# Optimization experiments

Measured on AMD Instinct MI355X. Metric: run time of the kernel, lower is better.

Reference implementation:

```python
import jax, jax.numpy as jnp
import numpy as np

HEADS = 8
NEG_SLOPE = 0.2


def _leaky(x):
    return jnp.where(x >= 0, x, NEG_SLOPE * x)


def _layernorm(x, g, b):
    # torch nn.LayerNorm over last dim, eps=1e-5, biased variance
    m = x.mean(-1, keepdims=True)
    v = ((x - m) ** 2).mean(-1, keepdims=True)
    return (x - m) / jnp.sqrt(v + 1e-5) * g + b


def _batchnorm(x, g, b):
    # training-mode BatchNorm2d, eps=1e-4, biased variance over (N,H,W)
    m = x.mean((0, 2, 3), keepdims=True)
    v = ((x - m) ** 2).mean((0, 2, 3), keepdims=True)
    return (x - m) / jnp.sqrt(v + 1e-4) * g[None, :, None, None] + b[None, :, None, None]


def _depthwise3x3(x, k):
    # x: (B,C,H,W), k: (C,1,3,3) depthwise kernel
    C = x.shape[1]
    return jax.lax.conv_general_dilated(
        x, k, (1, 1), 'SAME', feature_group_count=C,
        dimension_numbers=('NCHW', 'OIHW', 'NCHW'))


def _attn_layer(x, wq, wk, wv, wproj, bproj, wpos):
    # x: (B,H,W,C) channels-last; MDTA-style transposed attention
    b, H, W, C = x.shape
    d = C // HEADS
    xf = x.reshape(b, H * W, C)
    q, k, v = xf @ wq, xf @ wk, xf @ wv  # (b, n, C)

    def split(t):
        return t.reshape(b, H * W, HEADS, d).transpose(0, 2, 3, 1)  # (b, h, d, n)

    qh, kh, vh = split(q), split(k), split(v)
    # F.normalize over token axis n (eps=1e-12)
    qn = qh / jnp.maximum(jnp.sqrt((qh * qh).sum(-1, keepdims=True)), 1e-12)
    kn = kh / jnp.maximum(jnp.sqrt((kh * kh).sum(-1, keepdims=True)), 1e-12)
    attn = jax.nn.softmax(jnp.einsum('bhdn,bhen->bhde', kn, qn), axis=-1)  # (b,h,d,d)
    o = jnp.einsum('bhde,bhen->bhdn', attn, vh)  # (b,h,d,n)
    o = o.transpose(0, 3, 1, 2).reshape(b, H * W, C)
    out_c = (o @ wproj + bproj).reshape(b, H, W, C)
    out_p = _depthwise3x3(v.reshape(b, H, W, C).transpose(0, 3, 1, 2), wpos).transpose(0, 2, 3, 1)
    return out_c * out_p


def _transformer_block(x, wq, wk, wv, wproj, bproj, wpos, ln_g, ln_b, wff):
    # x: NCHW -> BHWC, 2 (attn + prenorm-FF) residual blocks, -> NCHW
    x = x.transpose(0, 2, 3, 1)
    for i in range(wq.shape[0]):
        x = _attn_layer(x, wq[i], wk[i], wv[i], wproj[i], bproj[i], wpos[i]) + x
        x = _layernorm(x, ln_g[i], ln_b[i]) @ wff[i] + x
    return x.transpose(0, 3, 1, 2)


def _saa(x, w1, w2):
    # SAA_Block: 8x8 spatial pool, global min-max norm, bmm correlation, SE gating
    b, c, H, W = x.shape
    y = x.reshape(b, c, 8, H // 8, 8, W // 8).mean((3, 5)).reshape(b, c, 64)
    y = (y - y.min()) / (y.max() - y.min())
    y = jnp.einsum('bci,bdi->bcd', y, y).mean(2)[:, :, None, None]  # (b,c,1,1)
    g = (x * y).mean((2, 3))  # (b,c) global avg pool
    g = jax.nn.sigmoid(_leaky(g @ w1) @ w2)
    return x * g[:, :, None, None]


def setup_inputs() -> dict:
    key = jax.random.key(0)
    B, C, H, W = 16, 64, 128, 128
    L = 2  # num_blocks in Transformer_block
    ks = jax.random.split(key, 12)
    s = 0.05
    inp = {
        'x': jax.random.normal(ks[0], (B, C, H, W), jnp.float32),
        'wq': jax.random.normal(ks[1], (L, C, C), jnp.float32) * s,
        'wk': jax.random.normal(ks[2], (L, C, C), jnp.float32) * s,
        'wv': jax.random.normal(ks[3], (L, C, C), jnp.float32) * s,
        'wproj': jax.random.normal(ks[4], (L, C, C), jnp.float32) * s,
        'bproj': jnp.zeros((L, C), jnp.float32),
        'wpos': jax.random.normal(ks[5], (L, C, 1, 3, 3), jnp.float32) * s,
        'ln_g': jnp.ones((L, C), jnp.float32),
        'ln_b': jnp.zeros((L, C), jnp.float32),
        'wff': jax.random.normal(ks[6], (L, C, C), jnp.float32) * s,
        'bn1_g': jnp.ones((C,), jnp.float32),
        'bn1_b': jnp.zeros((C,), jnp.float32),
        'wd': jax.random.normal(ks[7], (C, C), jnp.float32) * s,
        'bn2_g': jnp.ones((C,), jnp.float32),
        'bn2_b': jnp.zeros((C,), jnp.float32),
        'saa_w1': jax.random.normal(ks[8], (C, C // 16), jnp.float32) * s,
        'saa_w2': jax.random.normal(ks[9], (C // 16, C), jnp.float32) * s,
    }
    return inp


def reference(x, wq, wk, wv, wproj, bproj, wpos, ln_g, ln_b, wff,
              bn1_g, bn1_b, wd, bn2_g, bn2_b, saa_w1, saa_w2):
    # res path: C (Transformer_block) -> L -> B -> D (1x1 conv) -> L -> B
    r = _transformer_block(x, wq, wk, wv, wproj, bproj, wpos, ln_g, ln_b, wff)
    r = _batchnorm(_leaky(r), bn1_g, bn1_b)
    r = jnp.einsum('bchw,co->bohw', r, wd)  # 1x1 conv, bias=False
    r = _batchnorm(_leaky(r), bn2_g, bn2_b)
    return _saa(r + x, saa_w1, saa_w2)
```

## Files before the change

kernel.cpp:

```cpp
#include <hip/hip_runtime.h>

constexpr int NB = 16, NC = 64, NH = 128, NW = 128;
constexpr int NPIX = NH * NW;
constexpr int NTOT = NB * NPIX;
constexpr size_t BUF = (size_t)NTOT * NC;

constexpr size_t OFF_A   = 0;
constexpr size_t OFF_ACT = BUF;
constexpr size_t OFF_V   = 2 * BUF;
constexpr size_t OFF_S   = 3 * BUF;
constexpr size_t OFF_QSQ = OFF_S   + 2*16*512;
constexpr size_t OFF_KSQ = OFF_QSQ + 2048;
constexpr size_t OFF_BN1 = OFF_KSQ + 2048;
constexpr size_t OFF_BN2 = OFF_BN1 + 128;
constexpr size_t ZERO_FLOATS = 16384 + 2048 + 2048 + 128 + 128;
constexpr size_t OFF_W2  = OFF_BN2 + 128;
constexpr size_t OFF_AB1 = OFF_W2  + 131072;
constexpr size_t OFF_AB2 = OFF_AB1 + 128;
constexpr size_t OFF_Y   = OFF_AB2 + 128;
constexpr size_t OFF_GATE= OFF_Y   + 65536;

__device__ __forceinline__ float leaky(float x) { return x >= 0.f ? x : 0.2f * x; }
#define RFL __builtin_amdgcn_readfirstlane

__global__ __launch_bounds__(256) void k_transpose_in(const float* __restrict__ x,
                                                      float* __restrict__ A) {
  __shared__ float t[64][65];
  int blk = blockIdx.x;
  int b = blk >> 8;
  int p0 = (blk & 255) * 64;
  int tid = threadIdx.x;
  int cq = tid >> 6, p = tid & 63;
  for (int i = 0; i < 16; i++) {
    int c = cq * 16 + i;
    t[p][c] = x[((size_t)(b * 64 + c)) * NPIX + p0 + p];
  }
  __syncthreads();
  int pq = tid >> 6, c = tid & 63;
  for (int i = 0; i < 16; i++) {
    int p2 = pq * 16 + i;
    A[((size_t)(b * NPIX + p0 + p2)) * 64 + c] = t[p2][c];
  }
}

__global__ __launch_bounds__(256, 2) void k_qkv(const float* __restrict__ act,
    const float* __restrict__ wq, const float* __restrict__ wk,
    const float* __restrict__ wv, float* __restrict__ v,
    float* __restrict__ S, float* __restrict__ qsq, float* __restrict__ ksq,
    int l) {
  __shared__ float xb[8][64];
  int tid = threadIdx.x;
  int lane = tid & 63;
  int wid = RFL((int)(blockIdx.x * 4 + (tid >> 6)));
  int wslot = wid & 3;
  int b = wid >> 8;
  const float* Wq = wq + (size_t)l * 4096;
  const float* Wk = wk + (size_t)l * 4096;
  const float* Wv = wv + (size_t)l * 4096;
  float wqc[64], wkc[64], wvc[64];
#pragma unroll
  for (int ci = 0; ci < 64; ci++) {
    wqc[ci] = Wq[ci * 64 + lane];
    wkc[ci] = Wk[ci * 64 + lane];
    wvc[ci] = Wv[ci * 64 + lane];
  }
  float Sacc[8];
#pragma unroll
  for (int e = 0; e < 8; e++) Sacc[e] = 0.f;
  float qsa = 0.f, ksa = 0.f;
  int gbase = lane & 56;
  int base = wid * 4096;
#pragma unroll 1
  for (int p = 0; p < 64; p++) {
    int off = base + p * 64;
    float xl = act[off + lane];
    int xs = wslot * 2 + (p & 1);
    xb[xs][lane] = xl;
    const float4* x4p = (const float4*)xb[xs];
    float q = 0.f, k = 0.f, vv = 0.f;
#pragma unroll
    for (int i = 0; i < 16; i++) {
      float4 x4 = x4p[i];
      q  = fmaf(x4.x, wqc[4*i+0], q);
      k  = fmaf(x4.x, wkc[4*i+0], k);
      vv = fmaf(x4.x, wvc[4*i+0], vv);
      q  = fmaf(x4.y, wqc[4*i+1], q);
      k  = fmaf(x4.y, wkc[4*i+1], k);
      vv = fmaf(x4.y, wvc[4*i+1], vv);
      q  = fmaf(x4.z, wqc[4*i+2], q);
      k  = fmaf(x4.z, wkc[4*i+2], k);
      vv = fmaf(x4.z, wvc[4*i+2], vv);
      q  = fmaf(x4.w, wqc[4*i+3], q);
      k  = fmaf(x4.w, wkc[4*i+3], k);
      vv = fmaf(x4.w, wvc[4*i+3], vv);
    }
    qsa = fmaf(q, q, qsa);
    ksa = fmaf(k, k, ksa);
#pragma unroll
    for (int e = 0; e < 8; e++) {
      float qe = __shfl(q, gbase + e, 64);
      Sacc[e] = fmaf(k, qe, Sacc[e]);
    }
    v[off + lane] = vv;
  }
  float* Sb = S + ((size_t)l * 16 + b) * 512 + lane * 8;
#pragma unroll
  for (int e = 0; e < 8; e++) atomicAdd(Sb + e, Sacc[e]);
  atomicAdd(qsq + ((size_t)l * 16 + b) * 64 + lane, qsa);
  atomicAdd(ksq + ((size_t)l * 16 + b) * 64 + lane, ksa);
}

__global__ __launch_bounds__(64) void k_attn(const float* __restrict__ S,
    const float* __restrict__ qsq, const float* __restrict__ ksq,
    const float* __restrict__ wproj, float* __restrict__ W2, int l) {
  int b = blockIdx.x, t = threadIdx.x;
  __shared__ float A[8][8][8];
  const float* Sb = S + ((size_t)l * 16 + b) * 512;
  const float* qs = qsq + ((size_t)l * 16 + b) * 64;
  const float* ks = ksq + ((size_t)l * 16 + b) * 64;
  int h = t >> 3, d = t & 7;
  float kden = fmaxf(sqrtf(ks[h * 8 + d]), 1e-12f);
  float pre[8];
  float mx = -1e30f;
#pragma unroll
  for (int e = 0; e < 8; e++) {
    float qden = fmaxf(sqrtf(qs[h * 8 + e]), 1e-12f);
    pre[e] = Sb[(h * 8 + d) * 8 + e] / (kden * qden);
    mx = fmaxf(mx, pre[e]);
  }
  float sum = 0.f;
#pragma unroll
  for (int e = 0; e < 8; e++) { pre[e] = expf(pre[e] - mx); sum += pre[e]; }
  float inv = 1.f / sum;
#pragma unroll
  for (int e = 0; e < 8; e++) A[h][d][e] = pre[e] * inv;
  __syncthreads();
  int co = t;
  const float* wp = wproj + (size_t)l * 4096;
  float* W2b = W2 + ((size_t)l * 16 + b) * 4096;
#pragma unroll 1
  for (int cin = 0; cin < 64; cin++) {
    int hh2 = cin >> 3, e = cin & 7;
    float acc = 0.f;
#pragma unroll
    for (int dd = 0; dd < 8; dd++)
      acc = fmaf(A[hh2][dd][e], wp[(hh2 * 8 + dd) * 64 + co], acc);
    W2b[cin * 64 + co] = acc;
  }
}

__global__ __launch_bounds__(256, 2) void k_attnout_ff(
    const float* __restrict__ vbuf, const float* __restrict__ actin,
    float* __restrict__ actout, const float* __restrict__ W2all,
    const float* __restrict__ bproj, const float* __restrict__ wpos,
    const float* __restrict__ lng, const float* __restrict__ lnb,
    const float* __restrict__ wff, float* __restrict__ bn1, int l, int dobn) {
  __shared__ float xb[8][64], yb[8][64];
  int tid = threadIdx.x;
  int lane = tid & 63;
  int bid = blockIdx.x;
  int sbid = (bid & 7) * 128 + (bid >> 3);
  int wid = RFL((int)(sbid * 4 + (tid >> 6)));
  int wslot = wid & 3;
  int b = wid >> 8;
  int widb = wid & 255;
  int hh = widb >> 1;
  int c0 = (widb & 1) * 64;
  const float* W2 = W2all + ((size_t)l * 16 + b) * 4096;
  const float* WF = wff + (size_t)l * 4096;
  float w2c[64], wfc[64];
#pragma unroll
  for (int ci = 0; ci < 64; ci++) {
    w2c[ci] = W2[ci * 64 + lane];
    wfc[ci] = WF[ci * 64 + lane];
  }
  float wpc[9];
#pragma unroll
  for (int kk = 0; kk < 9; kk++) wpc[kk] = wpos[(size_t)l * 576 + lane * 9 + kk];
  float bp = bproj[l * 64 + lane];
  float G  = lng[l * 64 + lane];
  float Bb = lnb[l * 64 + lane];

  bool okm = (hh > 0), okp = (hh < 127);
  int base = wid * 4096;
  float Lm = 0.f, L0 = 0.f, Lp = 0.f, Cm = 0.f, C0, Cp = 0.f;
  C0 = vbuf[base + lane];
  if (okm) Cm = vbuf[base - 8192 + lane];
  if (okp) Cp = vbuf[base + 8192 + lane];
  if (c0 == 64) {
    L0 = vbuf[base - 64 + lane];
    if (okm) Lm = vbuf[base - 64 - 8192 + lane];
    if (okp) Lp = vbuf[base - 64 + 8192 + lane];
  }
  float s_bn = 0.f, s2_bn = 0.f;
#pragma unroll 1
  for (int p = 0; p < 64; p++) {
    int off = base + p * 64;
    float Rm = 0.f, R0 = 0.f, Rp = 0.f;
    bool okc = (c0 + p + 1 < 128);
    if (okc) {
      R0 = vbuf[off + 64 + lane];
      if (okm) Rm = vbuf[off + 64 - 8192 + lane];
      if (okp) Rp = vbuf[off + 64 + 8192 + lane];
    }
    int xs = wslot * 2 + (p & 1);
    xb[xs][lane] = C0;
    const float4* x4p = (const float4*)xb[xs];
    float a0 = 0.f, a1 = 0.f, a2 = 0.f, a3 = 0.f;
#pragma unroll
    for (int i = 0; i < 16; i++) {
      float4 x4 = x4p[i];
      a0 = fmaf(x4.x, w2c[4*i+0], a0);
      a1 = fmaf(x4.y, w2c[4*i+1], a1);
      a2 = fmaf(x4.z, w2c[4*i+2], a2);
      a3 = fmaf(x4.w, w2c[4*i+3], a3);
    }
    float acc = (a0 + a1) + (a2 + a3) + bp;
    float op = Lm * wpc[0] + Cm * wpc[1] + Rm * wpc[2]
             + L0 * wpc[3] + C0 * wpc[4] + R0 * wpc[5]
             + Lp * wpc[6] + Cp * wpc[7] + Rp * wpc[8];
    float av = actin[off + lane];
    float y = acc * op + av;
    float t1 = y, t2 = y * y;
#pragma unroll
    for (int m = 1; m < 64; m <<= 1) {
      t1 += __shfl_xor(t1, m, 64);
      t2 += __shfl_xor(t2, m, 64);
    }
    float mean = t1 * (1.f / 64.f);
    float var = t2 * (1.f / 64.f) - mean * mean;
    float iv = 1.f / sqrtf(var + 1e-5f);
    float yn = (y - mean) * iv * G + Bb;
    yb[xs][lane] = yn;
    const float4* y4p = (const float4*)yb[xs];
    float o0 = 0.f, o1 = 0.f, o2 = 0.f, o3 = 0.f;
#pragma unroll
    for (int i = 0; i < 16; i++) {
      float4 y4 = y4p[i];
      o0 = fmaf(y4.x, wfc[4*i+0], o0);
      o1 = fmaf(y4.y, wfc[4*i+1], o1);
      o2 = fmaf(y4.z, wfc[4*i+2], o2);
      o3 = fmaf(y4.w, wfc[4*i+3], o3);
    }
    float out = y + (o0 + o1) + (o2 + o3);
    if (dobn) {
      float lo = leaky(out);
      s_bn += lo;
      s2_bn = fmaf(lo, lo, s2_bn);
    }
    actout[off + lane] = out;
    Lm = Cm; L0 = C0; Lp = Cp;
    Cm = Rm; C0 = R0; Cp = Rp;
  }
  if (dobn) {
    atomicAdd(&bn1[lane], s_bn);
    atomicAdd(&bn1[64 + lane], s2_bn);
  }
}

__global__ __launch_bounds__(64) void k_bnfin(const float* __restrict__ sums,
                                              const float* __restrict__ g,
                                              const float* __restrict__ bt,
                                              float* __restrict__ ab, float eps) {
  int c = threadIdx.x;
  float m = sums[c] * (1.f / (float)NTOT);
  float v = sums[64 + c] * (1.f / (float)NTOT) - m * m;
  float a = g[c] / sqrtf(v + eps);
  ab[c] = a;
  ab[64 + c] = bt[c] - m * a;
}

__global__ __launch_bounds__(256, 4) void k_conv1x1(const float* __restrict__ act,
    const float* __restrict__ ab, const float* __restrict__ wd,
    float* __restrict__ outv, float* __restrict__ bn2) {
  __shared__ float xb[8][64];
  int tid = threadIdx.x;
  int lane = tid & 63;
  int wid = RFL((int)(blockIdx.x * 4 + (tid >> 6)));
  int wslot = wid & 3;
  float wdc[64];
#pragma unroll
  for (int ci = 0; ci < 64; ci++) wdc[ci] = wd[ci * 64 + lane];
  float a1l = ab[lane], b1l = ab[64 + lane];
  float s_bn = 0.f, s2_bn = 0.f;
  int base = wid * 4096;
#pragma unroll 1
  for (int p = 0; p < 64; p++) {
    int off = base + p * 64;
    float xl = act[off + lane];
    float tl = fmaf(a1l, leaky(xl), b1l);
    int xs = wslot * 2 + (p & 1);
    xb[xs][lane] = tl;
    const float4* x4p = (const float4*)xb[xs];
    float a0 = 0.f, a1 = 0.f, a2 = 0.f, a3 = 0.f;
#pragma unroll
    for (int i = 0; i < 16; i++) {
      float4 x4 = x4p[i];
      a0 = fmaf(x4.x, wdc[4*i+0], a0);
      a1 = fmaf(x4.y, wdc[4*i+1], a1);
      a2 = fmaf(x4.z, wdc[4*i+2], a2);
      a3 = fmaf(x4.w, wdc[4*i+3], a3);
    }
    float out = leaky((a0 + a1) + (a2 + a3));
    s_bn += out;
    s2_bn = fmaf(out, out, s2_bn);
    outv[off + lane] = out;
  }
  atomicAdd(&bn2[lane], s_bn);
  atomicAdd(&bn2[64 + lane], s2_bn);
}

__global__ __launch_bounds__(512) void k_pool(const float* __restrict__ lr2,
    const float* __restrict__ xA, const float* __restrict__ ab2,
    float* __restrict__ y) {
  int blk = blockIdx.x;
  int b = blk >> 4;
  int br = (blk >> 1) & 7;
  int half = blk & 1;
  int t = threadIdx.x;
  int c = t & 63;
  int w8 = t >> 6;
  float a2 = ab2[c], b2 = ab2[64 + c];
  float acc[4];
#pragma unroll
  for (int i = 0; i < 4; i++) acc[i] = 0.f;
#pragma unroll 1
  for (int r = 0; r < 16; r++) {
    size_t base = ((size_t)(b * NPIX + (br * 16 + r) * NW + half * 64)) * 64;
#pragma unroll
    for (int i = 0; i < 8; i++) {
      size_t idx = base + (size_t)i * 512 + t;
      float sv = fmaf(a2, lr2[idx], b2) + xA[idx];
      acc[i >> 1] += sv;
    }
  }
  __shared__ float red[8][4][64];
#pragma unroll
  for (int i = 0; i < 4; i++) red[w8][i][c] = acc[i];
  __syncthreads();
  if (t < 256) {
    int bin = t >> 6, c2 = t & 63;
    float s = 0.f;
#pragma unroll
    for (int w = 0; w < 8; w++) s += red[w][bin][c2];
    y[((size_t)(b * 64 + c2)) * 64 + br * 8 + half * 4 + bin] = s * (1.f / 256.f);
  }
}

__global__ __launch_bounds__(1024) void k_saa(const float* __restrict__ y,
    const float* __restrict__ w1, const float* __restrict__ w2,
    float* __restrict__ gate) {
  int t = threadIdx.x;
  __shared__ float rmin[1024], rmax[1024];
  float mn = 1e30f, mx = -1e30f;
#pragma unroll 1
  for (int i = 0; i < 64; i++) {
    float vv = y[(size_t)i * 1024 + t];
    mn = fminf(mn, vv);
    mx = fmaxf(mx, vv);
  }
  rmin[t] = mn; rmax[t] = mx;
  __syncthreads();
  for (int s = 512; s > 0; s >>= 1) {
    if (t < s) {
      rmin[t] = fminf(rmin[t], rmin[t + s]);
      rmax[t] = fmaxf(rmax[t], rmax[t + s]);
    }
    __syncthreads();
  }
  float gmn = rmin[0], gmx = rmax[0];
  float inv = 1.f / (gmx - gmn);
  __syncthreads();
  int b = t >> 6;
  int i6 = t & 63;
  __shared__ float tl[16][64];
  {
    const float* yb2 = y + (size_t)b * 4096;
    float s = 0.f;
#pragma unroll 1
    for (int cl = 0; cl < 64; cl++) s += yb2[cl * 64 + i6];
    tl[b][i6] = (s - 64.f * gmn) * inv;
  }
  __syncthreads();
  int cc = i6;
  const float* yc = y + (size_t)b * 4096 + cc * 64;
  float z = 0.f, ms = 0.f;
#pragma unroll 1
  for (int ii = 0; ii < 64; ii++) {
    float yr = yc[ii];
    z = fmaf((yr - gmn) * inv, tl[b][ii], z);
    ms += yr;
  }
  z *= (1.f / 64.f);
  ms *= (1.f / 64.f);
  __shared__ float g0l[16][64];
  g0l[b][cc] = z * ms;
  __syncthreads();
  __shared__ float hl[16][4];
  if (t < 64) {
    int bb = t >> 2, j = t & 3;
    float h = 0.f;
#pragma unroll 1
    for (int c2 = 0; c2 < 64; c2++) h = fmaf(g0l[bb][c2], w1[c2 * 4 + j], h);
    hl[bb][j] = leaky(h);
  }
  __syncthreads();
  float acc = 0.f;
#pragma unroll
  for (int j = 0; j < 4; j++) acc = fmaf(hl[b][j], w2[j * 64 + cc], acc);
  gate[t] = 1.f / (1.f + expf(-acc));
}

__global__ __launch_bounds__(256) void k_out(const float* __restrict__ lr2,
    const float* __restrict__ xA, const float* __restrict__ ab2,
    const float* __restrict__ gate, float* __restrict__ out) {
  __shared__ float tile[64][65];
  int blk = blockIdx.x;
  int b = blk >> 8;
  int p0 = (blk & 255) * 64;
  int tid = threadIdx.x;
  int c = tid & 63, pq = tid >> 6;
  float a2 = ab2[c], b2 = ab2[64 + c];
  for (int i = 0; i < 16; i++) {
    int p = pq * 16 + i;
    size_t idx = ((size_t)(b * NPIX + p0 + p)) * 64 + c;
    tile[p][c] = fmaf(a2, lr2[idx], b2) + xA[idx];
  }
  __syncthreads();
  int p = tid & 63, cq = tid >> 6;
  for (int i = 0; i < 16; i++) {
    int c2 = cq * 16 + i;
    out[((size_t)(b * 64 + c2)) * NPIX + p0 + p] = tile[p][c2] * gate[b * 64 + c2];
  }
}

extern "C" void kernel_launch(void* const* d_in, const int* in_sizes, int n_in,
                              void* d_out, int out_size, void* d_ws, size_t ws_size,
                              hipStream_t stream) {
  const float* x     = (const float*)d_in[0];
  const float* wq    = (const float*)d_in[1];
  const float* wk    = (const float*)d_in[2];
  const float* wv    = (const float*)d_in[3];
  const float* wproj = (const float*)d_in[4];
  const float* bproj = (const float*)d_in[5];
  const float* wpos  = (const float*)d_in[6];
  const float* ln_g  = (const float*)d_in[7];
  const float* ln_b  = (const float*)d_in[8];
  const float* wff   = (const float*)d_in[9];
  const float* bn1_g = (const float*)d_in[10];
  const float* bn1_b = (const float*)d_in[11];
  const float* wd    = (const float*)d_in[12];
  const float* bn2_g = (const float*)d_in[13];
  const float* bn2_b = (const float*)d_in[14];
  const float* sw1   = (const float*)d_in[15];
  const float* sw2   = (const float*)d_in[16];

  float* ws   = (float*)d_ws;
  float* A    = ws + OFF_A;
  float* ACT  = ws + OFF_ACT;
  float* V    = ws + OFF_V;
  float* S    = ws + OFF_S;
  float* QSQ  = ws + OFF_QSQ;
  float* KSQ  = ws + OFF_KSQ;
  float* BN1S = ws + OFF_BN1;
  float* BN2S = ws + OFF_BN2;
  float* W2   = ws + OFF_W2;
  float* AB1  = ws + OFF_AB1;
  float* AB2  = ws + OFF_AB2;
  float* Y    = ws + OFF_Y;
  float* GATE = ws + OFF_GATE;

  hipMemsetAsync((void*)S, 0, ZERO_FLOATS * sizeof(float), stream);

  k_transpose_in<<<4096, 256, 0, stream>>>(x, A);

  for (int l = 0; l < 2; l++) {
    const float* in = (l == 0) ? A : ACT;
    k_qkv<<<1024, 256, 0, stream>>>(in, wq, wk, wv, V, S, QSQ, KSQ, l);
    k_attn<<<16, 64, 0, stream>>>(S, QSQ, KSQ, wproj, W2, l);
    k_attnout_ff<<<1024, 256, 0, stream>>>(V, in, ACT, W2, bproj, wpos,
                                           ln_g, ln_b, wff, BN1S, l, l == 1);
  }

  k_bnfin<<<1, 64, 0, stream>>>(BN1S, bn1_g, bn1_b, AB1, 1e-4f);
  k_conv1x1<<<1024, 256, 0, stream>>>(ACT, AB1, wd, V, BN2S);
  k_bnfin<<<1, 64, 0, stream>>>(BN2S, bn2_g, bn2_b, AB2, 1e-4f);
  k_pool<<<256, 512, 0, stream>>>(V, A, AB2, Y);
  k_saa<<<1, 1024, 0, stream>>>(Y, sw1, sw2, GATE);
  k_out<<<4096, 256, 0, stream>>>(V, A, AB2, GATE, (float*)d_out);
}
```

Before: 1.321 ms.

## Split QKV kernel into QK and V kernels, prefetch next rows, swizzle blocks

The fused QKV projection kernel is split into a Q/K kernel that accumulates attention statistics and a separate V projection kernel. Each needs fewer weight registers, so the V kernel can run at higher occupancy. Several streaming kernels now software-prefetch the next pixel row from global memory, and block indices are swizzled across XCDs. Occupancy hints switch to amdgpu_waves_per_eu. The cost is that the activation input is now read twice per layer.

```diff
diff --git a/kernel.cpp b/kernel.cpp
--- a/kernel.cpp
+++ b/kernel.cpp
@@ -22,6 +22,7 @@
 
 __device__ __forceinline__ float leaky(float x) { return x >= 0.f ? x : 0.2f * x; }
 #define RFL __builtin_amdgcn_readfirstlane
+#define WAVES_EU(mn, mx) __attribute__((amdgpu_waves_per_eu(mn, mx)))
 
 __global__ __launch_bounds__(256) void k_transpose_in(const float* __restrict__ x,
                                                       float* __restrict__ A) {
@@ -43,26 +44,26 @@
   }
 }
 
-__global__ __launch_bounds__(256, 2) void k_qkv(const float* __restrict__ act,
+__global__ __launch_bounds__(256) WAVES_EU(2, 2) void k_qk(
+    const float* __restrict__ act,
     const float* __restrict__ wq, const float* __restrict__ wk,
-    const float* __restrict__ wv, float* __restrict__ v,
     float* __restrict__ S, float* __restrict__ qsq, float* __restrict__ ksq,
     int l) {
   __shared__ float xb[8][64];
   int tid = threadIdx.x;
   int lane = tid & 63;
-  int wid = RFL((int)(blockIdx.x * 4 + (tid >> 6)));
-  int wslot = wid & 3;
+  int bid = blockIdx.x;
+  int sbid = (bid & 7) * 128 + (bid >> 3);
+  int wid = RFL((int)(sbid * 4 + (tid >> 6)));
+  int wslot = (tid >> 6) & 3;
   int b = wid >> 8;
   const float* Wq = wq + (size_t)l * 4096;
   const float* Wk = wk + (size_t)l * 4096;
-  const float* Wv = wv + (size_t)l * 4096;
-  float wqc[64], wkc[64], wvc[64];
+  float wqc[64], wkc[64];
 #pragma unroll
   for (int ci = 0; ci < 64; ci++) {
     wqc[ci] = Wq[ci * 64 + lane];
     wkc[ci] = Wk[ci * 64 + lane];
-    wvc[ci] = Wv[ci * 64 + lane];
   }
   float Sacc[8];
 #pragma unroll
@@ -70,29 +71,27 @@
   float qsa = 0.f, ksa = 0.f;
   int gbase = lane & 56;
   int base = wid * 4096;
+  float xl = act[base + lane];
 #pragma unroll 1
   for (int p = 0; p < 64; p++) {
     int off = base + p * 64;
-    float xl = act[off + lane];
     int xs = wslot * 2 + (p & 1);
     xb[xs][lane] = xl;
+    float xn = 0.f;
+    if (p < 63) xn = act[off + 64 + lane];
     const float4* x4p = (const float4*)xb[xs];
-    float q = 0.f, k = 0.f, vv = 0.f;
+    float q = 0.f, k = 0.f;
 #pragma unroll
     for (int i = 0; i < 16; i++) {
       float4 x4 = x4p[i];
-      q  = fmaf(x4.x, wqc[4*i+0], q);
-      k  = fmaf(x4.x, wkc[4*i+0], k);
-      vv = fmaf(x4.x, wvc[4*i+0], vv);
-      q  = fmaf(x4.y, wqc[4*i+1], q);
-      k  = fmaf(x4.y, wkc[4*i+1], k);
-      vv = fmaf(x4.y, wvc[4*i+1], vv);
-      q  = fmaf(x4.z, wqc[4*i+2], q);
-      k  = fmaf(x4.z, wkc[4*i+2], k);
-      vv = fmaf(x4.z, wvc[4*i+2], vv);
-      q  = fmaf(x4.w, wqc[4*i+3], q);
-      k  = fmaf(x4.w, wkc[4*i+3], k);
-      vv = fmaf(x4.w, wvc[4*i+3], vv);
+      q = fmaf(x4.x, wqc[4*i+0], q);
+      k = fmaf(x4.x, wkc[4*i+0], k);
+      q = fmaf(x4.y, wqc[4*i+1], q);
+      k = fmaf(x4.y, wkc[4*i+1], k);
+      q = fmaf(x4.z, wqc[4*i+2], q);
+      k = fmaf(x4.z, wkc[4*i+2], k);
+      q = fmaf(x4.w, wqc[4*i+3], q);
+      k = fmaf(x4.w, wkc[4*i+3], k);
     }
     qsa = fmaf(q, q, qsa);
     ksa = fmaf(k, k, ksa);
@@ -101,13 +100,51 @@
       float qe = __shfl(q, gbase + e, 64);
       Sacc[e] = fmaf(k, qe, Sacc[e]);
     }
-    v[off + lane] = vv;
+    xl = xn;
   }
   float* Sb = S + ((size_t)l * 16 + b) * 512 + lane * 8;
 #pragma unroll
   for (int e = 0; e < 8; e++) atomicAdd(Sb + e, Sacc[e]);
   atomicAdd(qsq + ((size_t)l * 16 + b) * 64 + lane, qsa);
   atomicAdd(ksq + ((size_t)l * 16 + b) * 64 + lane, ksa);
+}
+
+__global__ __launch_bounds__(256) WAVES_EU(4, 4) void k_mat_v(
+    const float* __restrict__ act, const float* __restrict__ wv,
+    float* __restrict__ v, int l) {
+  __shared__ float xb[8][64];
+  int tid = threadIdx.x;
+  int lane = tid & 63;
+  int bid = blockIdx.x;
+  int sbid = (bid & 7) * 128 + (bid >> 3);
+  int wid = RFL((int)(sbid * 4 + (tid >> 6)));
+  int wslot = (tid >> 6) & 3;
+  const float* Wv = wv + (size_t)l * 4096;
+  float wvc[64];
+#pragma unroll
+  for (int ci = 0; ci < 64; ci++) wvc[ci] = Wv[ci * 64 + lane];
+  int base = wid * 4096;
+  float xl = act[base + lane];
+#pragma unroll 1
+  for (int p = 0; p < 64; p++) {
+    int off = base + p * 64;
+    int xs = wslot * 2 + (p & 1);
+    xb[xs][lane] = xl;
+    float xn = 0.f;
+    if (p < 63) xn = act[off + 64 + lane];
+    const float4* x4p = (const float4*)xb[xs];
+    float a0 = 0.f, a1 = 0.f, a2 = 0.f, a3 = 0.f;
+#pragma unroll
+    for (int i = 0; i < 16; i++) {
+      float4 x4 = x4p[i];
+      a0 = fmaf(x4.x, wvc[4*i+0], a0);
+      a1 = fmaf(x4.y, wvc[4*i+1], a1);
+      a2 = fmaf(x4.z, wvc[4*i+2], a2);
+      a3 = fmaf(x4.w, wvc[4*i+3], a3);
+    }
+    v[off + lane] = (a0 + a1) + (a2 + a3);
+    xl = xn;
+  }
 }
 
 __global__ __launch_bounds__(64) void k_attn(const float* __restrict__ S,
@@ -149,7 +186,7 @@
   }
 }
 
-__global__ __launch_bounds__(256, 2) void k_attnout_ff(
+__global__ __launch_bounds__(256) WAVES_EU(2, 2) void k_attnout_ff(
     const float* __restrict__ vbuf, const float* __restrict__ actin,
     float* __restrict__ actout, const float* __restrict__ W2all,
     const float* __restrict__ bproj, const float* __restrict__ wpos,
@@ -161,7 +198,7 @@
   int bid = blockIdx.x;
   int sbid = (bid & 7) * 128 + (bid >> 3);
   int wid = RFL((int)(sbid * 4 + (tid >> 6)));
-  int wslot = wid & 3;
+  int wslot = (tid >> 6) & 3;
   int b = wid >> 8;
   int widb = wid & 255;
   int hh = widb >> 1;
@@ -192,17 +229,19 @@
     if (okm) Lm = vbuf[base - 64 - 8192 + lane];
     if (okp) Lp = vbuf[base - 64 + 8192 + lane];
   }
+  float av = actin[base + lane];
   float s_bn = 0.f, s2_bn = 0.f;
 #pragma unroll 1
   for (int p = 0; p < 64; p++) {
     int off = base + p * 64;
-    float Rm = 0.f, R0 = 0.f, Rp = 0.f;
+    float Rm = 0.f, R0 = 0.f, Rp = 0.f, avn = 0.f;
     bool okc = (c0 + p + 1 < 128);
     if (okc) {
       R0 = vbuf[off + 64 + lane];
       if (okm) Rm = vbuf[off + 64 - 8192 + lane];
       if (okp) Rp = vbuf[off + 64 + 8192 + lane];
     }
+    if (p < 63) avn = actin[off + 64 + lane];
     int xs = wslot * 2 + (p & 1);
     xb[xs][lane] = C0;
     const float4* x4p = (const float4*)xb[xs];
@@ -219,7 +258,6 @@
     float op = Lm * wpc[0] + Cm * wpc[1] + Rm * wpc[2]
              + L0 * wpc[3] + C0 * wpc[4] + R0 * wpc[5]
              + Lp * wpc[6] + Cp * wpc[7] + Rp * wpc[8];
-    float av = actin[off + lane];
     float y = acc * op + av;
     float t1 = y, t2 = y * y;
 #pragma unroll
@@ -251,6 +289,7 @@
     actout[off + lane] = out;
     Lm = Cm; L0 = C0; Lp = Cp;
     Cm = Rm; C0 = R0; Cp = Rp;
+    av = avn;
   }
   if (dobn) {
     atomicAdd(&bn1[lane], s_bn);
@@ -270,27 +309,32 @@
   ab[64 + c] = bt[c] - m * a;
 }
 
-__global__ __launch_bounds__(256, 4) void k_conv1x1(const float* __restrict__ act,
+__global__ __launch_bounds__(256) WAVES_EU(4, 4) void k_conv1x1(
+    const float* __restrict__ act,
     const float* __restrict__ ab, const float* __restrict__ wd,
     float* __restrict__ outv, float* __restrict__ bn2) {
   __shared__ float xb[8][64];
   int tid = threadIdx.x;
   int lane = tid & 63;
-  int wid = RFL((int)(blockIdx.x * 4 + (tid >> 6)));
-  int wslot = wid & 3;
+  int bid = blockIdx.x;
+  int sbid = (bid & 7) * 128 + (bid >> 3);
+  int wid = RFL((int)(sbid * 4 + (tid >> 6)));
+  int wslot = (tid >> 6) & 3;
   float wdc[64];
 #pragma unroll
   for (int ci = 0; ci < 64; ci++) wdc[ci] = wd[ci * 64 + lane];
   float a1l = ab[lane], b1l = ab[64 + lane];
   float s_bn = 0.f, s2_bn = 0.f;
   int base = wid * 4096;
+  float xl = act[base + lane];
 #pragma unroll 1
   for (int p = 0; p < 64; p++) {
     int off = base + p * 64;
-    float xl = act[off + lane];
     float tl = fmaf(a1l, leaky(xl), b1l);
     int xs = wslot * 2 + (p & 1);
     xb[xs][lane] = tl;
+    float xn = 0.f;
+    if (p < 63) xn = act[off + 64 + lane];
     const float4* x4p = (const float4*)xb[xs];
     float a0 = 0.f, a1 = 0.f, a2 = 0.f, a3 = 0.f;
 #pragma unroll
@@ -305,6 +349,7 @@
     s_bn += out;
     s2_bn = fmaf(out, out, s2_bn);
     outv[off + lane] = out;
+    xl = xn;
   }
   atomicAdd(&bn2[lane], s_bn);
   atomicAdd(&bn2[64 + lane], s2_bn);
@@ -476,7 +521,8 @@
 
   for (int l = 0; l < 2; l++) {
     const float* in = (l == 0) ? A : ACT;
-    k_qkv<<<1024, 256, 0, stream>>>(in, wq, wk, wv, V, S, QSQ, KSQ, l);
+    k_qk<<<1024, 256, 0, stream>>>(in, wq, wk, S, QSQ, KSQ, l);
+    k_mat_v<<<1024, 256, 0, stream>>>(in, wv, V, l);
     k_attn<<<16, 64, 0, stream>>>(S, QSQ, KSQ, wproj, W2, l);
     k_attnout_ff<<<1024, 256, 0, stream>>>(V, in, ACT, W2, bproj, wpos,
                                            ln_g, ln_b, wff, BN1S, l, l == 1);
```

Measured after the change: 1.331 ms. Within noise of the previous version (+0.7%).
